# Kernel optimization log

Measured on AMD Instinct MI355X. Metric: run time of the kernel, lower is better.

The kernel has to match this reference:

```python
import jax, jax.numpy as jnp
import numpy as np

B, T, E, H, L = 32, 2048, 256, 256, 2


def setup_inputs() -> dict:
    key = jax.random.key(0)
    k = jax.random.split(key, 6)
    x = jax.random.normal(k[0], (B, T, E), jnp.float32)
    h0 = jax.random.normal(k[1], (L, B, H), jnp.float32)
    # weights scaled to avoid tanh saturation (mimics fan-in init)
    W0 = jax.random.normal(k[2], (E + H, H), jnp.float32) * 0.05
    b0 = jax.random.normal(k[3], (H,), jnp.float32) * 0.05
    W1 = jax.random.normal(k[4], (2 * H, H), jnp.float32) * 0.05
    b1 = jax.random.normal(k[5], (H,), jnp.float32) * 0.05
    return {"x": x, "h0": h0, "W0": W0, "b0": b0, "W1": W1, "b1": b1}


def reference(x, h0, W0, b0, W1, b1):
    # x: [B,T,E]; h0: [L,B,H] (torch permutes to [B,L,H])
    h_init = jnp.transpose(h0, (1, 0, 2))  # [B,L,H]
    Ws = (W0, W1)
    bs = (b0, b1)

    def step(h, x_t):  # h: [B,L,H], x_t: [B,E]
        inp = x_t
        new_h = []
        for l in range(L):  # small fixed stack of cells
            z = jnp.concatenate([inp, h[:, l, :]], axis=-1) @ Ws[l] + bs[l]
            ht = jnp.tanh(z)  # [B,H]
            inp = ht
            new_h.append(ht)
        return jnp.stack(new_h, axis=1), ht  # carry, per-step top-layer output

    x_tbe = jnp.transpose(x, (1, 0, 2))  # [T,B,E]
    h_final, outs = jax.lax.scan(step, h_init, x_tbe)
    hidden_states = jnp.transpose(outs, (1, 0, 2))  # [B,T,H]
    ht = h_final[:, -1:, :]  # final top-layer state, [B,1,H]
    return hidden_states, ht
```

## Files before the change

### kernel.cpp

```cpp
#include <hip/hip_runtime.h>


typedef _Float16 half2_t __attribute__((ext_vector_type(2)));

#define TT 2048
#define BB 32
#define XPB 8
#define CHUNK 64
#define NCHUNK (TT / CHUNK)

__device__ __forceinline__ unsigned packw(float lo, float hi) {
    half2_t r;
    r.x = (_Float16)lo;
    r.y = (_Float16)hi;
    return __builtin_bit_cast(unsigned, r);
}
#define H2(X) __builtin_bit_cast(half2_t, (X))

#define LDS_BARRIER() asm volatile("s_waitcnt lgkmcnt(0)\n\ts_barrier" ::: "memory")

__device__ __forceinline__ int rload(int* pf) {
    return __hip_atomic_load(pf, __ATOMIC_RELAXED, __HIP_MEMORY_SCOPE_AGENT);
}
__device__ __forceinline__ void astore(int* pf, int v) {
    __hip_atomic_store(pf, v, __ATOMIC_RELEASE, __HIP_MEMORY_SCOPE_AGENT);
}
#define ACQUIRE_FENCE() __builtin_amdgcn_fence(__ATOMIC_ACQUIRE, "agent")

#define KAW8(B)                                                             \
    "+v"(wp[(B)]), "+v"(wp[(B) + 1]), "+v"(wp[(B) + 2]), "+v"(wp[(B) + 3]), \
    "+v"(wp[(B) + 4]), "+v"(wp[(B) + 5]), "+v"(wp[(B) + 6]), "+v"(wp[(B) + 7])
#define KEEPALIVE()                                                  \
    asm volatile("" : KAW8(0), KAW8(8), KAW8(16), KAW8(24));         \
    asm volatile("" : KAW8(32), KAW8(40), KAW8(48), KAW8(56));       \
    asm volatile("" : KAW8(64), KAW8(72), KAW8(80), KAW8(88));       \
    asm volatile("" : KAW8(96), KAW8(104), KAW8(112), KAW8(120));

#define FDOT(H, W_, A) A = __builtin_amdgcn_fdot2(H2(H), H2(W_), A, false)
#define FD4(H, K)               \
    FDOT(H, wp[(K)], ac0);      \
    FDOT(H, wp[32 + (K)], ac1); \
    FDOT(H, wp[64 + (K)], ac2); \
    FDOT(H, wp[96 + (K)], ac3);

#define DOTS()                                                          \
    float ac0 = 0.f, ac1 = 0.f, ac2 = 0.f, ac3 = 0.f;                   \
    {                                                                   \
        const uint4* hp_ = hbq + 9 * p;                                 \
        uint4 q0 = hp_[0], q1 = hp_[1], q2 = hp_[2], q3 = hp_[3];       \
        uint4 q4 = hp_[4], q5 = hp_[5], q6 = hp_[6], q7 = hp_[7];       \
        FD4(q0.x, 0)  FD4(q0.y, 1)  FD4(q0.z, 2)  FD4(q0.w, 3)         \
        FD4(q1.x, 4)  FD4(q1.y, 5)  FD4(q1.z, 6)  FD4(q1.w, 7)         \
        FD4(q2.x, 8)  FD4(q2.y, 9)  FD4(q2.z, 10) FD4(q2.w, 11)        \
        FD4(q3.x, 12) FD4(q3.y, 13) FD4(q3.z, 14) FD4(q3.w, 15)        \
        FD4(q4.x, 16) FD4(q4.y, 17) FD4(q4.z, 18) FD4(q4.w, 19)        \
        FD4(q5.x, 20) FD4(q5.y, 21) FD4(q5.z, 22) FD4(q5.w, 23)        \
        FD4(q6.x, 24) FD4(q6.y, 25) FD4(q6.z, 26) FD4(q6.w, 27)        \
        FD4(q7.x, 28) FD4(q7.y, 29) FD4(q7.z, 30) FD4(q7.w, 31)        \
    }

#define BFLY(x)                                                              \
    asm("v_add_f32_dpp %0, %0, %0 quad_perm:[1,0,3,2] row_mask:0xf "         \
        "bank_mask:0xf"                                                      \
        : "+v"(x));                                                          \
    asm("v_add_f32_dpp %0, %0, %0 quad_perm:[2,3,0,1] row_mask:0xf "         \
        "bank_mask:0xf"                                                      \
        : "+v"(x));

#define LOAD_WP4(Wm, rowbase, p_, jg_)                                       \
    _Pragma("unroll")                                                        \
    for (int c = 0; c < 4; ++c) {                                            \
        _Pragma("unroll")                                                    \
        for (int k = 0; k < 32; ++k) {                                       \
            const int col_ = (jg_) + 64 * c;                                 \
            wp[c * 32 + k] =                                                 \
                packw((Wm)[(size_t)((rowbase) + 64 * (p_) + 2 * k) * 256 +   \
                           col_],                                            \
                      (Wm)[(size_t)((rowbase) + 64 * (p_) + 2 * k + 1) * 256 \
                           + col_]);                                         \
        }                                                                    \
    }

__device__ __forceinline__ int sidx_of(int i) {
    return 72 * (i >> 6) + (i & 63);
}

template <bool ALIAS>
__device__ __forceinline__ void proj_rows(
    const float* __restrict__ src, float* __restrict__ dst,
    unsigned (&wp)[128], float bj, int nrows, uint4 (*hb)[36], int tid,
    int p, int jg, int col)
{
    _Float16* st0 = reinterpret_cast<_Float16*>(hb[0]);
    _Float16* st1 = reinterpret_cast<_Float16*>(hb[1]);
    const int si = sidx_of(tid);
    st0[si] = (_Float16)src[tid];
    __syncthreads();
    for (int r = 0; r < nrows; ++r) {
        KEEPALIVE()
        _Float16* stn = (r & 1) ? st0 : st1;
        if (r + 1 < nrows) stn[si] = (_Float16)src[(size_t)(r + 1) * 256 + tid];
        const uint4* hbq = hb[r & 1];
        DOTS()
        BFLY(ac0) BFLY(ac1) BFLY(ac2) BFLY(ac3)
        float z = (p == 0) ? ac0 : ((p == 1) ? ac1 : ((p == 2) ? ac2 : ac3));
        dst[(size_t)r * 256 + col] = z + bj;
        if (ALIAS) __syncthreads();
        else LDS_BARRIER();
    }
}

template <int MODE>
__device__ __forceinline__ void scan_core(
    const float* __restrict__ W, const float* __restrict__ h_init,
    const float* __restrict__ xsrc, float* __restrict__ hdst, float* hfinal,
    int* pubflag, int* waitflags, uint4 (*hb)[36], int tid)
{
    const int p = tid & 3;
    const int jg = tid >> 2;
    const int col = jg + 64 * p;

    unsigned wp[128];
    LOAD_WP4(W, 256, p, jg)

    _Float16* hw0 = reinterpret_cast<_Float16*>(hb[0]);
    _Float16* hw1 = reinterpret_cast<_Float16*>(hb[1]);
    hw0[sidx_of(tid)] = (_Float16)h_init[tid];
    const int wsi = 72 * p + jg;

    float xpc[XPB], xpn[XPB], hs[XPB];

    auto step = [&](int t, float xp) -> float {
        KEEPALIVE()
        const uint4* hbq = hb[t & 1];
        DOTS()
        BFLY(ac0) BFLY(ac1) BFLY(ac2) BFLY(ac3)
        float z = (p == 0) ? ac0 : ((p == 1) ? ac1 : ((p == 2) ? ac2 : ac3));
        z += xp;
        const float e = __expf(2.0f * z);
        const float hn = 1.0f - 2.0f / (e + 1.0f);
        _Float16* dstw = ((t + 1) & 1) ? hw1 : hw0;
        dstw[wsi] = (_Float16)hn;
        LDS_BARRIER();
        return hn;
    };

    if (MODE != 2) {
#pragma unroll
        for (int u = 0; u < XPB; ++u) xpc[u] = xsrc[(size_t)u * 256 + col];
        __syncthreads();
        for (int t0 = 0; t0 < TT; t0 += XPB) {
            const bool more = (t0 + XPB) < TT;
            if (more) {
#pragma unroll
                for (int u = 0; u < XPB; ++u)
                    xpn[u] = xsrc[(size_t)(t0 + XPB + u) * 256 + col];
            }
#pragma unroll
            for (int u = 0; u < XPB; ++u) hs[u] = step(t0 + u, xpc[u]);
#pragma unroll
            for (int u = 0; u < XPB; ++u)
                hdst[(size_t)(t0 + u) * 256 + col] = hs[u];
            if (MODE == 1 && (((t0 + XPB) & (CHUNK - 1)) == 0)) {
                __syncthreads();
                if (tid == 0) astore(pubflag, t0 + XPB);
            }
            if (more) {
#pragma unroll
                for (int u = 0; u < XPB; ++u) xpc[u] = xpn[u];
            }
        }
        if (MODE == 0 && hfinal != nullptr) hfinal[col] = hs[XPB - 1];
    } else {
        __syncthreads();
        for (int chunk = 0; chunk < NCHUNK; ++chunk) {
            const int tbase = chunk * CHUNK;
            while (rload(&waitflags[chunk]) == 0) __builtin_amdgcn_s_sleep(1);
            ACQUIRE_FENCE();
#pragma unroll
            for (int u = 0; u < XPB; ++u)
                xpc[u] = xsrc[(size_t)(tbase + u) * 256 + col];
            for (int g = 0; g < CHUNK / XPB; ++g) {
                const int t0 = tbase + g * XPB;
                if (g + 1 < CHUNK / XPB) {
#pragma unroll
                    for (int u = 0; u < XPB; ++u)
                        xpn[u] = xsrc[(size_t)(t0 + XPB + u) * 256 + col];
                }
#pragma unroll
                for (int u = 0; u < XPB; ++u) hs[u] = step(t0 + u, xpc[u]);
#pragma unroll
                for (int u = 0; u < XPB; ++u)
                    hdst[(size_t)(t0 + u) * 256 + col] = hs[u];
                if (t0 + XPB == TT) hfinal[col] = hs[XPB - 1];
                if (g + 1 < CHUNK / XPB) {
#pragma unroll
                    for (int u = 0; u < XPB; ++u) xpc[u] = xpn[u];
                }
            }
        }
    }
}

template <bool ALIAS>
__global__ __launch_bounds__(256, 1) void proj21_kernel(
    const float* in, const float* __restrict__ W, const float* __restrict__ bias,
    float* out, int rows_per_wg)
{
    __shared__ uint4 hb[2][36];
    const int tid = threadIdx.x;
    const int p = tid & 3;
    const int jg = tid >> 2;
    const int col = jg + 64 * p;
    unsigned wp[128];
    LOAD_WP4(W, 0, p, jg)
    const float bj = bias[col];
    const size_t r0 = (size_t)blockIdx.x * rows_per_wg;
    proj_rows<ALIAS>(in + r0 * 256, out + r0 * 256, wp, bj, rows_per_wg, hb,
                     tid, p, jg, col);
}

__global__ __launch_bounds__(256, 1) void scan21_kernel(
    const float* __restrict__ W, const float* __restrict__ h_init,
    float* __restrict__ io, float* __restrict__ hfinal)
{
    __shared__ uint4 hb[2][36];
    const int b = blockIdx.x;
    scan_core<0>(W, h_init + b * 256, io + (size_t)b * TT * 256,
                 io + (size_t)b * TT * 256,
                 hfinal ? hfinal + b * 256 : nullptr, nullptr, nullptr, hb,
                 threadIdx.x);
}

__global__ __launch_bounds__(256, 1) void mega21_kernel(
    const float* __restrict__ W0, const float* __restrict__ W1,
    const float* __restrict__ b1v, const float* __restrict__ h0init,
    float* xpA, float* out, int* flags)
{
    __shared__ uint4 hb[2][36];
    const int tid = threadIdx.x;
    const int bid = blockIdx.x;
    int* flagL0 = flags;
    int* chunkdone = flags + BB * 16;

    if (bid < BB) {
        const int b = bid;
        scan_core<1>(W0, h0init + b * 256, xpA + (size_t)b * TT * 256,
                     out + (size_t)b * TT * 256, nullptr, &flagL0[b * 16],
                     nullptr, hb, tid);
    } else if (bid >= 3 * BB) {
        const int b = bid - 3 * BB;
        scan_core<2>(W1, h0init + (size_t)(BB + b) * 256,
                     xpA + (size_t)b * TT * 256, out + (size_t)b * TT * 256,
                     out + (size_t)BB * TT * 256 + b * 256, nullptr,
                     &chunkdone[b * NCHUNK], hb, tid);
    } else {
        const int k = bid - BB;
        const int b = k >> 1;
        const int half = k & 1;
        const int p = tid & 3;
        const int jg = tid >> 2;
        const int col = jg + 64 * p;

        unsigned wp[128];
        LOAD_WP4(W1, 0, p, jg)
        const float bj = b1v[col];

        for (int chunk = half; chunk < NCHUNK; chunk += 2) {
            while (rload(&flagL0[b * 16]) < (chunk + 1) * CHUNK)
                __builtin_amdgcn_s_sleep(1);
            ACQUIRE_FENCE();
            const int tbase = chunk * CHUNK;
            const float* src = out + ((size_t)b * TT + tbase) * 256;
            float* dst = xpA + ((size_t)b * TT + tbase) * 256;
            proj_rows<false>(src, dst, wp, bj, CHUNK, hb, tid, p, jg, col);
            __syncthreads();
            if (tid == 0) astore(&chunkdone[b * NCHUNK + chunk], 1);
        }
    }
}

extern "C" void kernel_launch(void* const* d_in, const int* in_sizes, int n_in,
                              void* d_out, int out_size, void* d_ws, size_t ws_size,
                              hipStream_t stream) {
    const float* x  = (const float*)d_in[0];
    const float* h0 = (const float*)d_in[1];
    const float* W0 = (const float*)d_in[2];
    const float* b0 = (const float*)d_in[3];
    const float* W1 = (const float*)d_in[4];
    const float* b1 = (const float*)d_in[5];
    float* out = (float*)d_out;

    const size_t XPA_FLOATS = (size_t)BB * TT * 256;
    const size_t FLAG_INTS = (size_t)BB * 16 + (size_t)BB * NCHUNK;
    const size_t NEEDED = XPA_FLOATS * 4 + FLAG_INTS * 4;

    if (ws_size >= NEEDED) {
        float* xpA = (float*)d_ws;
        int* flags = (int*)((char*)d_ws + XPA_FLOATS * 4);
        hipMemsetAsync(flags, 0, FLAG_INTS * 4, stream);
        proj21_kernel<false><<<512, 256, 0, stream>>>(x, W0, b0, xpA, 128);
        mega21_kernel<<<4 * BB, 256, 0, stream>>>(W0, W1, b1, h0, xpA, out, flags);
    } else {
        proj21_kernel<true><<<512, 256, 0, stream>>>(x, W0, b0, out, 128);
        scan21_kernel<<<BB, 256, 0, stream>>>(W0, h0, out, nullptr);
        proj21_kernel<true><<<512, 256, 0, stream>>>(out, W1, b1, out, 128);
        scan21_kernel<<<BB, 256, 0, stream>>>(W1, h0 + BB * 256, out, out + XPA_FLOATS);
    }
}
```

Baseline: 1.228 ms.

## Split recurrent dot across 8 lanes per output with contiguous column ownership

The recurrent scan step now splits each hidden column's 256-long dot product across 8 lanes of 32 elements instead of 4 lanes of 64. Each thread owns 8 adjacent columns, so there are 8 accumulators and a 3-stage DPP butterfly including a row_half_mirror. Each lane reads only 4 uint4 of h from LDS per step instead of 8, and the output column becomes the thread id, which gives coalesced global stores. The cost is more accumulator registers, an extra DPP reduction stage per accumulator, and a longer select chain. The padded LDS row stride changes from 72 to 40.

```diff
diff --git a/kernel.cpp b/kernel.cpp
--- a/kernel.cpp
+++ b/kernel.cpp
@@ -37,6 +37,7 @@
     asm volatile("" : KAW8(96), KAW8(104), KAW8(112), KAW8(120));
 
 #define FDOT(H, W_, A) A = __builtin_amdgcn_fdot2(H2(H), H2(W_), A, false)
+
 #define FD4(H, K)               \
     FDOT(H, wp[(K)], ac0);      \
     FDOT(H, wp[32 + (K)], ac1); \
@@ -67,6 +68,12 @@
         "bank_mask:0xf"                                                      \
         : "+v"(x));
 
+#define BFLY8(x)                                                             \
+    BFLY(x)                                                                  \
+    asm("v_add_f32_dpp %0, %0, %0 row_half_mirror row_mask:0xf "             \
+        "bank_mask:0xf"                                                      \
+        : "+v"(x));
+
 #define LOAD_WP4(Wm, rowbase, p_, jg_)                                       \
     _Pragma("unroll")                                                        \
     for (int c = 0; c < 4; ++c) {                                            \
@@ -81,14 +88,53 @@
         }                                                                    \
     }
 
+#define FD8(H, D)               \
+    FDOT(H, wp[(D)], ac0);      \
+    FDOT(H, wp[16 + (D)], ac1); \
+    FDOT(H, wp[32 + (D)], ac2); \
+    FDOT(H, wp[48 + (D)], ac3); \
+    FDOT(H, wp[64 + (D)], ac4); \
+    FDOT(H, wp[80 + (D)], ac5); \
+    FDOT(H, wp[96 + (D)], ac6); \
+    FDOT(H, wp[112 + (D)], ac7);
+
+#define DOTS8()                                                         \
+    float ac0 = 0.f, ac1 = 0.f, ac2 = 0.f, ac3 = 0.f;                   \
+    float ac4 = 0.f, ac5 = 0.f, ac6 = 0.f, ac7 = 0.f;                   \
+    {                                                                   \
+        const uint4* hp_ = hbq + 5 * le;                                \
+        uint4 q0 = hp_[0], q1 = hp_[1], q2 = hp_[2], q3 = hp_[3];       \
+        FD8(q0.x, 0)  FD8(q0.y, 1)  FD8(q0.z, 2)  FD8(q0.w, 3)         \
+        FD8(q1.x, 4)  FD8(q1.y, 5)  FD8(q1.z, 6)  FD8(q1.w, 7)         \
+        FD8(q2.x, 8)  FD8(q2.y, 9)  FD8(q2.z, 10) FD8(q2.w, 11)        \
+        FD8(q3.x, 12) FD8(q3.y, 13) FD8(q3.z, 14) FD8(q3.w, 15)        \
+    }
+
+#define LOAD_WP8(Wm, rowbase, le_, jg_)                                      \
+    _Pragma("unroll")                                                        \
+    for (int c = 0; c < 8; ++c) {                                            \
+        _Pragma("unroll")                                                    \
+        for (int d = 0; d < 16; ++d) {                                       \
+            const int col_ = 8 * (jg_) + c;                                  \
+            wp[c * 16 + d] =                                                 \
+                packw((Wm)[(size_t)((rowbase) + 32 * (le_) + 2 * d) * 256 +  \
+                           col_],                                            \
+                      (Wm)[(size_t)((rowbase) + 32 * (le_) + 2 * d + 1) *    \
+                               256 + col_]);                                 \
+        }                                                                    \
+    }
+
 __device__ __forceinline__ int sidx_of(int i) {
     return 72 * (i >> 6) + (i & 63);
+}
+__device__ __forceinline__ int sidx8_of(int i) {
+    return 40 * (i >> 5) + (i & 31);
 }
 
 template <bool ALIAS>
 __device__ __forceinline__ void proj_rows(
     const float* __restrict__ src, float* __restrict__ dst,
-    unsigned (&wp)[128], float bj, int nrows, uint4 (*hb)[36], int tid,
+    unsigned (&wp)[128], float bj, int nrows, uint4 (*hb)[40], int tid,
     int p, int jg, int col)
 {
     _Float16* st0 = reinterpret_cast<_Float16*>(hb[0]);
@@ -114,31 +160,38 @@
 __device__ __forceinline__ void scan_core(
     const float* __restrict__ W, const float* __restrict__ h_init,
     const float* __restrict__ xsrc, float* __restrict__ hdst, float* hfinal,
-    int* pubflag, int* waitflags, uint4 (*hb)[36], int tid)
-{
-    const int p = tid & 3;
-    const int jg = tid >> 2;
-    const int col = jg + 64 * p;
+    int* pubflag, int* waitflags, uint4 (*hb)[40], int tid)
+{
+    const int le = tid & 7;
+    const int jg = tid >> 3;
+    const int col = tid;
 
     unsigned wp[128];
-    LOAD_WP4(W, 256, p, jg)
+    LOAD_WP8(W, 256, le, jg)
 
     _Float16* hw0 = reinterpret_cast<_Float16*>(hb[0]);
     _Float16* hw1 = reinterpret_cast<_Float16*>(hb[1]);
-    hw0[sidx_of(tid)] = (_Float16)h_init[tid];
-    const int wsi = 72 * p + jg;
+    hw0[sidx8_of(tid)] = (_Float16)h_init[tid];
+    const int wsi = sidx8_of(col);
 
     float xpc[XPB], xpn[XPB], hs[XPB];
 
     auto step = [&](int t, float xp) -> float {
         KEEPALIVE()
         const uint4* hbq = hb[t & 1];
-        DOTS()
-        BFLY(ac0) BFLY(ac1) BFLY(ac2) BFLY(ac3)
-        float z = (p == 0) ? ac0 : ((p == 1) ? ac1 : ((p == 2) ? ac2 : ac3));
+        DOTS8()
+        BFLY8(ac0) BFLY8(ac1) BFLY8(ac2) BFLY8(ac3)
+        BFLY8(ac4) BFLY8(ac5) BFLY8(ac6) BFLY8(ac7)
+        float z = (le == 0) ? ac0
+                : (le == 1) ? ac1
+                : (le == 2) ? ac2
+                : (le == 3) ? ac3
+                : (le == 4) ? ac4
+                : (le == 5) ? ac5
+                : (le == 6) ? ac6 : ac7;
         z += xp;
-        const float e = __expf(2.0f * z);
-        const float hn = 1.0f - 2.0f / (e + 1.0f);
+        const float ex = __expf(2.0f * z);
+        const float hn = 1.0f - 2.0f / (ex + 1.0f);
         _Float16* dstw = ((t + 1) & 1) ? hw1 : hw0;
         dstw[wsi] = (_Float16)hn;
         LDS_BARRIER();
@@ -203,11 +256,11 @@
 }
 
 template <bool ALIAS>
-__global__ __launch_bounds__(256, 1) void proj21_kernel(
+__global__ __launch_bounds__(256, 1) void proj22_kernel(
     const float* in, const float* __restrict__ W, const float* __restrict__ bias,
     float* out, int rows_per_wg)
 {
-    __shared__ uint4 hb[2][36];
+    __shared__ uint4 hb[2][40];
     const int tid = threadIdx.x;
     const int p = tid & 3;
     const int jg = tid >> 2;
@@ -220,11 +273,11 @@
                      tid, p, jg, col);
 }
 
-__global__ __launch_bounds__(256, 1) void scan21_kernel(
+__global__ __launch_bounds__(256, 1) void scan22_kernel(
     const float* __restrict__ W, const float* __restrict__ h_init,
     float* __restrict__ io, float* __restrict__ hfinal)
 {
-    __shared__ uint4 hb[2][36];
+    __shared__ uint4 hb[2][40];
     const int b = blockIdx.x;
     scan_core<0>(W, h_init + b * 256, io + (size_t)b * TT * 256,
                  io + (size_t)b * TT * 256,
@@ -232,12 +285,12 @@
                  threadIdx.x);
 }
 
-__global__ __launch_bounds__(256, 1) void mega21_kernel(
+__global__ __launch_bounds__(256, 1) void mega22_kernel(
     const float* __restrict__ W0, const float* __restrict__ W1,
     const float* __restrict__ b1v, const float* __restrict__ h0init,
     float* xpA, float* out, int* flags)
 {
-    __shared__ uint4 hb[2][36];
+    __shared__ uint4 hb[2][40];
     const int tid = threadIdx.x;
     const int bid = blockIdx.x;
     int* flagL0 = flags;
@@ -299,12 +352,12 @@
         float* xpA = (float*)d_ws;
         int* flags = (int*)((char*)d_ws + XPA_FLOATS * 4);
         hipMemsetAsync(flags, 0, FLAG_INTS * 4, stream);
-        proj21_kernel<false><<<512, 256, 0, stream>>>(x, W0, b0, xpA, 128);
-        mega21_kernel<<<4 * BB, 256, 0, stream>>>(W0, W1, b1, h0, xpA, out, flags);
+        proj22_kernel<false><<<512, 256, 0, stream>>>(x, W0, b0, xpA, 128);
+        mega22_kernel<<<4 * BB, 256, 0, stream>>>(W0, W1, b1, h0, xpA, out, flags);
     } else {
-        proj21_kernel<true><<<512, 256, 0, stream>>>(x, W0, b0, out, 128);
-        scan21_kernel<<<BB, 256, 0, stream>>>(W0, h0, out, nullptr);
-        proj21_kernel<true><<<512, 256, 0, stream>>>(out, W1, b1, out, 128);
-        scan21_kernel<<<BB, 256, 0, stream>>>(W1, h0 + BB * 256, out, out + XPA_FLOATS);
-    }
-}
+        proj22_kernel<true><<<512, 256, 0, stream>>>(x, W0, b0, out, 128);
+        scan22_kernel<<<BB, 256, 0, stream>>>(W0, h0, out, nullptr);
+        proj22_kernel<true><<<512, 256, 0, stream>>>(out, W1, b1, out, 128);
+        scan22_kernel<<<BB, 256, 0, stream>>>(W1, h0 + BB * 256, out, out + XPA_FLOATS);
+    }
+}
```

Result: slower. 1.381 ms (+12.4%).

## Fuse layer-0 input projection into persistent mega kernel with per-chunk flags

Applied to the files above, without the earlier changes.

Removes the separate layer-0 input-projection launch. Instead, 64 extra blocks in the persistent kernel compute the projection chunk by chunk and publish a per-chunk flag. The layer-0 scan waits on those flags, so it can start as soon as its first chunk is ready rather than after the whole projection finishes. Scan control flow is unified into a WAIT/PUB templated loop. This adds flag polling, more resident blocks, and a dependence on all 192 blocks being co-resident.

```diff
diff --git a/kernel.cpp b/kernel.cpp
--- a/kernel.cpp
+++ b/kernel.cpp
@@ -110,7 +110,7 @@
     }
 }
 
-template <int MODE>
+template <bool WAIT, bool PUB>
 __device__ __forceinline__ void scan_core(
     const float* __restrict__ W, const float* __restrict__ h_init,
     const float* __restrict__ xsrc, float* __restrict__ hdst, float* hfinal,
@@ -145,13 +145,19 @@
         return hn;
     };
 
-    if (MODE != 2) {
-#pragma unroll
-        for (int u = 0; u < XPB; ++u) xpc[u] = xsrc[(size_t)u * 256 + col];
-        __syncthreads();
-        for (int t0 = 0; t0 < TT; t0 += XPB) {
-            const bool more = (t0 + XPB) < TT;
-            if (more) {
+    __syncthreads();
+    for (int chunk = 0; chunk < NCHUNK; ++chunk) {
+        const int tbase = chunk * CHUNK;
+        if (WAIT) {
+            while (rload(&waitflags[chunk]) == 0) __builtin_amdgcn_s_sleep(1);
+            ACQUIRE_FENCE();
+        }
+#pragma unroll
+        for (int u = 0; u < XPB; ++u)
+            xpc[u] = xsrc[(size_t)(tbase + u) * 256 + col];
+        for (int g = 0; g < CHUNK / XPB; ++g) {
+            const int t0 = tbase + g * XPB;
+            if (g + 1 < CHUNK / XPB) {
 #pragma unroll
                 for (int u = 0; u < XPB; ++u)
                     xpn[u] = xsrc[(size_t)(t0 + XPB + u) * 256 + col];
@@ -161,49 +167,21 @@
 #pragma unroll
             for (int u = 0; u < XPB; ++u)
                 hdst[(size_t)(t0 + u) * 256 + col] = hs[u];
-            if (MODE == 1 && (((t0 + XPB) & (CHUNK - 1)) == 0)) {
-                __syncthreads();
-                if (tid == 0) astore(pubflag, t0 + XPB);
-            }
-            if (more) {
+            if (t0 + XPB == TT && hfinal != nullptr) hfinal[col] = hs[XPB - 1];
+            if (g + 1 < CHUNK / XPB) {
 #pragma unroll
                 for (int u = 0; u < XPB; ++u) xpc[u] = xpn[u];
             }
         }
-        if (MODE == 0 && hfinal != nullptr) hfinal[col] = hs[XPB - 1];
-    } else {
-        __syncthreads();
-        for (int chunk = 0; chunk < NCHUNK; ++chunk) {
-            const int tbase = chunk * CHUNK;
-            while (rload(&waitflags[chunk]) == 0) __builtin_amdgcn_s_sleep(1);
-            ACQUIRE_FENCE();
-#pragma unroll
-            for (int u = 0; u < XPB; ++u)
-                xpc[u] = xsrc[(size_t)(tbase + u) * 256 + col];
-            for (int g = 0; g < CHUNK / XPB; ++g) {
-                const int t0 = tbase + g * XPB;
-                if (g + 1 < CHUNK / XPB) {
-#pragma unroll
-                    for (int u = 0; u < XPB; ++u)
-                        xpn[u] = xsrc[(size_t)(t0 + XPB + u) * 256 + col];
-                }
-#pragma unroll
-                for (int u = 0; u < XPB; ++u) hs[u] = step(t0 + u, xpc[u]);
-#pragma unroll
-                for (int u = 0; u < XPB; ++u)
-                    hdst[(size_t)(t0 + u) * 256 + col] = hs[u];
-                if (t0 + XPB == TT) hfinal[col] = hs[XPB - 1];
-                if (g + 1 < CHUNK / XPB) {
-#pragma unroll
-                    for (int u = 0; u < XPB; ++u) xpc[u] = xpn[u];
-                }
-            }
+        if (PUB) {
+            __syncthreads();
+            if (tid == 0) astore(pubflag, tbase + CHUNK);
         }
     }
 }
 
 template <bool ALIAS>
-__global__ __launch_bounds__(256, 1) void proj21_kernel(
+__global__ __launch_bounds__(256, 1) void proj23_kernel(
     const float* in, const float* __restrict__ W, const float* __restrict__ bias,
     float* out, int rows_per_wg)
 {
@@ -220,20 +198,21 @@
                      tid, p, jg, col);
 }
 
-__global__ __launch_bounds__(256, 1) void scan21_kernel(
+__global__ __launch_bounds__(256, 1) void scan23_kernel(
     const float* __restrict__ W, const float* __restrict__ h_init,
     float* __restrict__ io, float* __restrict__ hfinal)
 {
     __shared__ uint4 hb[2][36];
     const int b = blockIdx.x;
-    scan_core<0>(W, h_init + b * 256, io + (size_t)b * TT * 256,
-                 io + (size_t)b * TT * 256,
-                 hfinal ? hfinal + b * 256 : nullptr, nullptr, nullptr, hb,
-                 threadIdx.x);
-}
-
-__global__ __launch_bounds__(256, 1) void mega21_kernel(
-    const float* __restrict__ W0, const float* __restrict__ W1,
+    scan_core<false, false>(W, h_init + b * 256, io + (size_t)b * TT * 256,
+                            io + (size_t)b * TT * 256,
+                            hfinal ? hfinal + b * 256 : nullptr, nullptr,
+                            nullptr, hb, threadIdx.x);
+}
+
+__global__ __launch_bounds__(256, 1) void mega23_kernel(
+    const float* __restrict__ x, const float* __restrict__ W0,
+    const float* __restrict__ b0v, const float* __restrict__ W1,
     const float* __restrict__ b1v, const float* __restrict__ h0init,
     float* xpA, float* out, int* flags)
 {
@@ -242,19 +221,14 @@
     const int bid = blockIdx.x;
     int* flagL0 = flags;
     int* chunkdone = flags + BB * 16;
+    int* xp0done = flags + BB * 16 + BB * NCHUNK;
 
     if (bid < BB) {
         const int b = bid;
-        scan_core<1>(W0, h0init + b * 256, xpA + (size_t)b * TT * 256,
-                     out + (size_t)b * TT * 256, nullptr, &flagL0[b * 16],
-                     nullptr, hb, tid);
-    } else if (bid >= 3 * BB) {
-        const int b = bid - 3 * BB;
-        scan_core<2>(W1, h0init + (size_t)(BB + b) * 256,
-                     xpA + (size_t)b * TT * 256, out + (size_t)b * TT * 256,
-                     out + (size_t)BB * TT * 256 + b * 256, nullptr,
-                     &chunkdone[b * NCHUNK], hb, tid);
-    } else {
+        scan_core<true, true>(W0, h0init + b * 256, xpA + (size_t)b * TT * 256,
+                              out + (size_t)b * TT * 256, nullptr,
+                              &flagL0[b * 16], &xp0done[b * NCHUNK], hb, tid);
+    } else if (bid < 3 * BB) {
         const int k = bid - BB;
         const int b = k >> 1;
         const int half = k & 1;
@@ -277,6 +251,33 @@
             __syncthreads();
             if (tid == 0) astore(&chunkdone[b * NCHUNK + chunk], 1);
         }
+    } else if (bid < 4 * BB) {
+        const int b = bid - 3 * BB;
+        scan_core<true, false>(W1, h0init + (size_t)(BB + b) * 256,
+                               xpA + (size_t)b * TT * 256,
+                               out + (size_t)b * TT * 256,
+                               out + (size_t)BB * TT * 256 + b * 256, nullptr,
+                               &chunkdone[b * NCHUNK], hb, tid);
+    } else {
+        const int k = bid - 4 * BB;
+        const int b = k >> 1;
+        const int half = k & 1;
+        const int p = tid & 3;
+        const int jg = tid >> 2;
+        const int col = jg + 64 * p;
+
+        unsigned wp[128];
+        LOAD_WP4(W0, 0, p, jg)
+        const float bj = b0v[col];
+
+        for (int chunk = half; chunk < NCHUNK; chunk += 2) {
+            const int tbase = chunk * CHUNK;
+            const float* src = x + ((size_t)b * TT + tbase) * 256;
+            float* dst = xpA + ((size_t)b * TT + tbase) * 256;
+            proj_rows<false>(src, dst, wp, bj, CHUNK, hb, tid, p, jg, col);
+            __syncthreads();
+            if (tid == 0) astore(&xp0done[b * NCHUNK + chunk], 1);
+        }
     }
 }
 
@@ -292,19 +293,20 @@
     float* out = (float*)d_out;
 
     const size_t XPA_FLOATS = (size_t)BB * TT * 256;
-    const size_t FLAG_INTS = (size_t)BB * 16 + (size_t)BB * NCHUNK;
+    const size_t FLAG_INTS = (size_t)BB * 16 + 2 * (size_t)BB * NCHUNK;
     const size_t NEEDED = XPA_FLOATS * 4 + FLAG_INTS * 4;
 
     if (ws_size >= NEEDED) {
         float* xpA = (float*)d_ws;
         int* flags = (int*)((char*)d_ws + XPA_FLOATS * 4);
         hipMemsetAsync(flags, 0, FLAG_INTS * 4, stream);
-        proj21_kernel<false><<<512, 256, 0, stream>>>(x, W0, b0, xpA, 128);
-        mega21_kernel<<<4 * BB, 256, 0, stream>>>(W0, W1, b1, h0, xpA, out, flags);
+        mega23_kernel<<<6 * BB, 256, 0, stream>>>(x, W0, b0, W1, b1, h0, xpA,
+                                                  out, flags);
     } else {
-        proj21_kernel<true><<<512, 256, 0, stream>>>(x, W0, b0, out, 128);
-        scan21_kernel<<<BB, 256, 0, stream>>>(W0, h0, out, nullptr);
-        proj21_kernel<true><<<512, 256, 0, stream>>>(out, W1, b1, out, 128);
-        scan21_kernel<<<BB, 256, 0, stream>>>(W1, h0 + BB * 256, out, out + XPA_FLOATS);
-    }
-}
+        proj23_kernel<true><<<512, 256, 0, stream>>>(x, W0, b0, out, 128);
+        scan23_kernel<<<BB, 256, 0, stream>>>(W0, h0, out, nullptr);
+        proj23_kernel<true><<<512, 256, 0, stream>>>(out, W1, b1, out, 128);
+        scan23_kernel<<<BB, 256, 0, stream>>>(W1, h0 + BB * 256, out,
+                                              out + XPA_FLOATS);
+    }
+}
```

New measurement: 1.188 ms. 1.03x faster.
